# Kernel tuning notes

Measured on AMD Instinct MI355X. Metric: run time of the kernel, lower is better.

## Reference

```python
import jax, jax.numpy as jnp
import numpy as np

N = 100000   # nodes
E = 1600000  # edges
IN_DIM, HID, HEADS, OUT_DIM = 8, 64, 4, 3


def _add_self_loops(src, dst, n):
    loop = jnp.arange(n, dtype=src.dtype)
    return jnp.concatenate([src, loop]), jnp.concatenate([dst, loop])


def gcn_conv(x, src, dst, n, W, b):
    # PyG GCNConv: add self-loops, symmetric normalization deg^-1/2 * deg^-1/2
    s, d = _add_self_loops(src, dst, n)
    deg = jax.ops.segment_sum(jnp.ones(s.shape[0], x.dtype), d, num_segments=n)
    dinv = jnp.where(deg > 0, jax.lax.rsqrt(deg), 0.0)
    norm = dinv[s] * dinv[d]                       # [E']
    h = x @ W                                      # [N, out]
    out = jax.ops.segment_sum(norm[:, None] * h[s], d, num_segments=n)
    return out + b


def gat_conv(x, src, dst, n, W, att_src, att_dst, b):
    # PyG GATConv, concat=True, negative_slope=0.2, self-loops added
    h = (x @ W).reshape(n, HEADS, HID)             # [N, H, C]
    s, d = _add_self_loops(src, dst, n)
    a_src = jnp.sum(h * att_src, axis=-1)          # [N, H]
    a_dst = jnp.sum(h * att_dst, axis=-1)          # [N, H]
    e = jax.nn.leaky_relu(a_src[s] + a_dst[d], negative_slope=0.2)  # [E', H]
    m = jax.lax.stop_gradient(jax.ops.segment_max(e, d, num_segments=n))
    ex = jnp.exp(e - m[d])
    denom = jax.ops.segment_sum(ex, d, num_segments=n)
    alpha = ex / (denom[d] + 1e-16)                # segment softmax over incoming edges
    out = jax.ops.segment_sum(alpha[:, :, None] * h[s], d, num_segments=n)  # [N, H, C]
    return out.reshape(n, HEADS * HID) + b


def setup_inputs() -> dict:
    key = jax.random.key(0)
    ks = jax.random.split(key, 16)
    def glorot(k, shape):
        fan = shape[0] + shape[-1]
        return jax.random.normal(k, shape, jnp.float32) * np.sqrt(2.0 / fan)
    return {
        "x": jax.random.normal(ks[0], (N, IN_DIM), jnp.float32),
        "edge_index": jax.random.randint(ks[1], (2, E), 0, N, jnp.int64 if jax.config.jax_enable_x64 else jnp.int32),
        "w1": glorot(ks[2], (IN_DIM, HID)), "b1": jnp.zeros((HID,), jnp.float32),
        "w2": glorot(ks[3], (HID, HID)),   "b2": jnp.zeros((HID,), jnp.float32),
        "w3": glorot(ks[4], (HID, HID)),   "b3": jnp.zeros((HID,), jnp.float32),
        "wg": glorot(ks[5], (HID, HEADS * HID)), "bg": jnp.zeros((HEADS * HID,), jnp.float32),
        "att_src": glorot(ks[6], (HEADS, HID)),
        "att_dst": glorot(ks[7], (HEADS, HID)),
        "wc1": glorot(ks[8], (HEADS * HID, HID)), "bc1": jnp.zeros((HID,), jnp.float32),
        "wc2": glorot(ks[9], (HID, OUT_DIM)),     "bc2": jnp.zeros((OUT_DIM,), jnp.float32),
    }


def reference(x, edge_index, w1, b1, w2, b2, w3, b3, wg, bg, att_src, att_dst, wc1, bc1, wc2, bc2):
    src, dst = edge_index[0], edge_index[1]
    n = x.shape[0]
    # stacked GCN convs with ReLU; residual when shapes match (layers 2,3)
    h = jax.nn.relu(gcn_conv(x, src, dst, n, w1, b1))
    h = h + jax.nn.relu(gcn_conv(h, src, dst, n, w2, b2))
    h = h + jax.nn.relu(gcn_conv(h, src, dst, n, w3, b3))
    # GAT attention layer (4 heads, concat)
    h_att = gat_conv(h, src, dst, n, wg, att_src, att_dst, bg)  # [N, 256]
    # classifier MLP (dropout is inference no-op)
    z = jax.nn.relu(h_att @ wc1 + bc1)
    logits = z @ wc2 + bc2
    return jax.nn.log_softmax(logits, axis=1)
```

## Files before the change

kernel.cpp:

```cpp
#include <hip/hip_runtime.h>
#include <math.h>


typedef _Float16 half8 __attribute__((ext_vector_type(8)));
typedef _Float16 f16x8 __attribute__((ext_vector_type(8)));
typedef float f32x4 __attribute__((ext_vector_type(4)));

__device__ __forceinline__ float leaky02(float v) { return v > 0.f ? v : 0.2f * v; }


template <int CTRL>
__device__ __forceinline__ float dpp_add(float v) {
    int iv = __builtin_bit_cast(int, v);
    int r = __builtin_amdgcn_update_dpp(iv, iv, CTRL, 0xF, 0xF, false);
    return v + __builtin_bit_cast(float, r);
}
template <int OFF>
__device__ __forceinline__ float swz_add(float v) {
    int r = __builtin_amdgcn_ds_swizzle(__builtin_bit_cast(int, v), OFF);
    return v + __builtin_bit_cast(float, r);
}
template <int CTRL>
__device__ __forceinline__ float dpp_max(float v) {
    int iv = __builtin_bit_cast(int, v);
    int r = __builtin_amdgcn_update_dpp(iv, iv, CTRL, 0xF, 0xF, false);
    return fmaxf(v, __builtin_bit_cast(float, r));
}
template <int OFF>
__device__ __forceinline__ float swz_max(float v) {
    int r = __builtin_amdgcn_ds_swizzle(__builtin_bit_cast(int, v), OFF);
    return fmaxf(v, __builtin_bit_cast(float, r));
}
__device__ __forceinline__ float red8(float v) {
    v = dpp_add<0xB1>(v);
    v = dpp_add<0x4E>(v);
    v = swz_add<0x101F>(v);
    return v;
}
__device__ __forceinline__ float red16(float v) {
    v = dpp_add<0xB1>(v);
    v = dpp_add<0x4E>(v);
    v = swz_add<0x101F>(v);
    v = dpp_add<0x128>(v);
    return v;
}
__device__ __forceinline__ float red64(float v) {
    v = dpp_add<0xB1>(v);
    v = dpp_add<0x4E>(v);
    v = swz_add<0x101F>(v);
    v = dpp_add<0x128>(v);
    v = swz_add<0x401F>(v);
    v = v + __shfl_xor(v, 32);
    return v;
}
__device__ __forceinline__ float red64max(float v) {
    v = dpp_max<0xB1>(v);
    v = dpp_max<0x4E>(v);
    v = swz_max<0x101F>(v);
    v = dpp_max<0x128>(v);
    v = swz_max<0x401F>(v);
    v = fmaxf(v, __shfl_xor(v, 32));
    return v;
}


__global__ void count_kernel(const int* __restrict__ dst, int E, int range,
                             int* __restrict__ counts) {
    int grp = blockIdx.x & 7;
    int nlo = grp * range;
    int nhi = nlo + range;
    int nblk = gridDim.x >> 3;
    int c = blockIdx.x >> 3;
    int stride = nblk * blockDim.x;
    for (int e = c * blockDim.x + threadIdx.x; e < E; e += stride) {
        int d = dst[e];
        if (d >= nlo && d < nhi) atomicAdd(&counts[d], 1);
    }
}

__global__ void scan_pass1(const int* __restrict__ counts, int n, int* __restrict__ blockSums) {
    __shared__ int sh[256];
    int base = blockIdx.x * 2048;
    int tid = threadIdx.x;
    int s = 0;
#pragma unroll
    for (int j = 0; j < 8; ++j) {
        int idx = base + tid * 8 + j;
        if (idx < n) s += counts[idx];
    }
    sh[tid] = s;
    __syncthreads();
    for (int off = 128; off > 0; off >>= 1) {
        if (tid < off) sh[tid] += sh[tid + off];
        __syncthreads();
    }
    if (tid == 0) blockSums[blockIdx.x] = sh[0];
}

__global__ void scan_pass2(const int* __restrict__ blockSums, int nb, int* __restrict__ blockOffs) {
    if (threadIdx.x == 0 && blockIdx.x == 0) {
        int run = 0;
        for (int i = 0; i < nb; ++i) { blockOffs[i] = run; run += blockSums[i]; }
    }
}

__global__ void scan_pass3(const int* __restrict__ counts, int n,
                           const int* __restrict__ blockOffs,
                           const float* __restrict__ x,
                           int* __restrict__ row_ptr, int* __restrict__ cursor,
                           float* __restrict__ dinv, float* __restrict__ rdinv,
                           _Float16* __restrict__ xs) {
    __shared__ int sh[256];
    int base = blockIdx.x * 2048;
    int tid = threadIdx.x;
    int cnt[8];
    int local = 0;
#pragma unroll
    for (int j = 0; j < 8; ++j) {
        int idx = base + tid * 8 + j;
        cnt[j] = (idx < n) ? counts[idx] : 0;
        local += cnt[j];
    }
    sh[tid] = local;
    __syncthreads();
    for (int off = 1; off < 256; off <<= 1) {
        int v = (tid >= off) ? sh[tid - off] : 0;
        __syncthreads();
        sh[tid] += v;
        __syncthreads();
    }
    int run = blockOffs[blockIdx.x] + sh[tid] - local;
#pragma unroll
    for (int j = 0; j < 8; ++j) {
        int idx = base + tid * 8 + j;
        if (idx < n) {
            row_ptr[idx] = run;
            cursor[idx] = run;
            float dv = rsqrtf((float)(cnt[j] + 1));
            dinv[idx] = dv;
            rdinv[idx] = sqrtf((float)(cnt[j] + 1));
#pragma unroll
            for (int t = 0; t < 8; ++t) xs[idx * 8 + t] = (_Float16)(dv * x[idx * 8 + t]);
            run += cnt[j];
            if (idx == n - 1) row_ptr[n] = run;
        }
    }
}

__global__ void scatter_kernel(const int* __restrict__ src, const int* __restrict__ dst,
                               int E, int range,
                               int* __restrict__ cursor, int* __restrict__ col_src) {
    int grp = blockIdx.x & 7;
    int nlo = grp * range;
    int nhi = nlo + range;
    int nblk = gridDim.x >> 3;
    int c = blockIdx.x >> 3;
    int stride = nblk * blockDim.x;
    for (int e = c * blockDim.x + threadIdx.x; e < E; e += stride) {
        int d = dst[e];
        if (d >= nlo && d < nhi) {
            int pos = atomicAdd(&cursor[d], 1);
            col_src[pos] = src[e];
        }
    }
}


__global__ void ccomb_kernel(const float* __restrict__ Wg, const float* __restrict__ bg,
                             const float* __restrict__ wc1, const float* __restrict__ bc1,
                             const float* __restrict__ att_src, const float* __restrict__ att_dst,
                             const float* __restrict__ w2, const float* __restrict__ w3,
                             _Float16* __restrict__ CcombP, float* __restrict__ bcomb,
                             float* __restrict__ wse, float* __restrict__ wde,
                             _Float16* __restrict__ W2P, _Float16* __restrict__ W3P) {
    int bid = blockIdx.x;
    int j = threadIdx.x;
    if (bid < 256) {
        int i = bid;
        float s = 0.f;
        for (int c = 0; c < 64; ++c)
            s += Wg[(i & 63) * 256 + (i >> 6) * 64 + c] * wc1[((i >> 6) * 64 + c) * 64 + j];
        _Float16 hi = (_Float16)s;
        _Float16 lo = (_Float16)(s - (float)hi);
        int kt = i >> 5, l = (((i >> 3) & 3) << 4) | (j & 15), e = i & 7, ct = j >> 4;
        CcombP[(ct * 8 + kt) * 512 + l * 8 + e] = hi;
        CcombP[(32 + ct * 8 + kt) * 512 + l * 8 + e] = lo;
    } else if (bid == 256) {
        float s = bc1[j];
        for (int i = 0; i < 256; ++i) s += bg[i] * wc1[i * 64 + j];
        bcomb[j] = s;
#pragma unroll
        for (int h = 0; h < 4; ++h) {
            float ss = 0.f, sd = 0.f;
            for (int c = 0; c < 64; ++c) {
                float w = Wg[j * 256 + h * 64 + c];
                ss += w * att_src[h * 64 + c];
                sd += w * att_dst[h * 64 + c];
            }
            wse[j * 4 + h] = ss;
            wde[j * 4 + h] = sd;
        }
    } else {
        int i = (bid < 321) ? (bid - 257) : (bid - 321);
        const float* W = (bid < 321) ? w2 : w3;
        _Float16* WP = (bid < 321) ? W2P : W3P;
        float s = W[i * 64 + j];
        _Float16 hi = (_Float16)s;
        _Float16 lo = (_Float16)(s - (float)hi);
        int kt = i >> 5, l = (((i >> 3) & 3) << 4) | (j & 15), e = i & 7, ct = j >> 4;
        WP[(ct * 2 + kt) * 512 + l * 8 + e] = hi;
        WP[(8 + ct * 2 + kt) * 512 + l * 8 + e] = lo;
    }
}


__global__ void gcn_layer1(const half8* __restrict__ xs8,
                           const float* __restrict__ W1, const float* __restrict__ b1,
                           const int* __restrict__ row_ptr, const int* __restrict__ col_src,
                           const float* __restrict__ dinv, int n,
                           _Float16* __restrict__ hs1) {
    int tid = threadIdx.x, lane = tid & 63, wid = tid >> 6;
    int node = blockIdx.x * 4 + wid;
    if (node >= n) return;
    int beg = row_ptr[node], end = row_ptr[node + 1];
    int deg = end - beg;
    float acc[8] = {0.f, 0.f, 0.f, 0.f, 0.f, 0.f, 0.f, 0.f};
    for (int base = 0; base < deg; base += 64) {
        int cs = col_src[min(beg + base + lane, end - 1)];
        half8 v = xs8[cs];
        if (base + lane < deg) {
#pragma unroll
            for (int c = 0; c < 8; ++c) acc[c] += (float)v[c];
        }
    }
#pragma unroll
    for (int c = 0; c < 8; ++c) acc[c] = red64(acc[c]);
    half8 sv = xs8[node];
    float di = dinv[node];
    float agg[8];
#pragma unroll
    for (int c = 0; c < 8; ++c) agg[c] = (acc[c] + (float)sv[c]) * di;
    float sum = b1[lane];
#pragma unroll
    for (int k = 0; k < 8; ++k) sum = fmaf(agg[k], W1[k * 64 + lane], sum);
    hs1[node * 64 + lane] = (_Float16)(di * fmaxf(sum, 0.f));
}


__global__ void gcn_agg(const _Float16* __restrict__ hs_in,
                        const int* __restrict__ row_ptr, const int* __restrict__ col_src,
                        const float* __restrict__ dinv, int n,
                        _Float16* __restrict__ aggout) {
    int tid = threadIdx.x, lane = tid & 63, wid = tid >> 6;
    int node = blockIdx.x * 4 + wid;
    if (node >= n) return;
    int t = lane >> 3, g = lane & 7;
    const half8* hs8 = (const half8*)hs_in;
    int beg = row_ptr[node], end = row_ptr[node + 1];
    int deg = end - beg;
    half8 sv = hs8[node * 8 + t];
    float ac[8];
#pragma unroll
    for (int c = 0; c < 8; ++c) ac[c] = (g == 0) ? (float)sv[c] : 0.f;
    for (int base = 0; base < deg; base += 64) {
        int cs = col_src[min(beg + base + lane, end - 1)];
        int lim = min(deg - base, 64);
        auto bodyF = [&](int eo8) {
            int s = __shfl(cs, eo8 + g);
            half8 v = hs8[s * 8 + t];
#pragma unroll
            for (int c = 0; c < 8; ++c) ac[c] += (float)v[c];
        };
        auto bodyG = [&](int eo8) {
            int eo = eo8 + g;
            int s = __shfl(cs, eo);
            half8 v = hs8[s * 8 + t];
            if (eo < lim) {
#pragma unroll
                for (int c = 0; c < 8; ++c) ac[c] += (float)v[c];
            }
        };
        int eo8 = 0;
        for (; eo8 + 16 <= lim; eo8 += 16) { bodyF(eo8); bodyF(eo8 + 8); }
        if (eo8 < lim) {
            bodyG(eo8);
            eo8 += 8;
            if (eo8 < lim) bodyG(eo8);
        }
    }
    float di = dinv[node];
#pragma unroll
    for (int c = 0; c < 8; ++c) ac[c] = red8(ac[c]) * di;
    if (g == 0) {
        half8 hv;
#pragma unroll
        for (int c = 0; c < 8; ++c) hv[c] = (_Float16)ac[c];
        *(half8*)(aggout + (size_t)node * 64 + t * 8) = hv;
    }
}


template <bool LAST>
__global__ __launch_bounds__(256) void gcn_mfma(
        const _Float16* __restrict__ agg,
        const _Float16* __restrict__ WP,
        const float* __restrict__ b,
        const _Float16* __restrict__ hs_in,
        const float* __restrict__ dinv, const float* __restrict__ rdinv,
        const float* __restrict__ wse, const float* __restrict__ wde,
        int n, _Float16* __restrict__ hout,
        float4* __restrict__ a_src4, float4* __restrict__ a_dst4) {
    __shared__ float partS[4][16][4];
    __shared__ float partD[4][16][4];
    int tid = threadIdx.x;
    int lane = tid & 63;
    int w = __builtin_amdgcn_readfirstlane(tid >> 6);
    int c16 = lane & 15, hi = lane >> 4;

    f16x8 bh[2], blo[2];
#pragma unroll
    for (int kt = 0; kt < 2; ++kt) {
        bh[kt]  = *(const f16x8*)(WP + (size_t)(w * 2 + kt) * 512 + lane * 8);
        blo[kt] = *(const f16x8*)(WP + (size_t)(8 + w * 2 + kt) * 512 + lane * 8);
    }
    int col = w * 16 + c16;
    float bl = b[col];
    float4 wev, wdv;
    if (LAST) {
        wev = ((const float4*)wse)[col];
        wdv = ((const float4*)wde)[col];
    }

    int ntiles = (n + 15) >> 4;
    for (int tile = blockIdx.x; tile < ntiles; tile += gridDim.x) {
        int rowb = tile * 16;
        int arow = min(rowb + c16, n - 1);
        const _Float16* ap = agg + (size_t)arow * 64 + hi * 8;
        f16x8 a0 = *(const f16x8*)(ap);
        f16x8 a1 = *(const f16x8*)(ap + 32);
        f32x4 acc = {0.f, 0.f, 0.f, 0.f};
        acc = __builtin_amdgcn_mfma_f32_16x16x32_f16(a0, bh[0],  acc, 0, 0, 0);
        acc = __builtin_amdgcn_mfma_f32_16x16x32_f16(a0, blo[0], acc, 0, 0, 0);
        acc = __builtin_amdgcn_mfma_f32_16x16x32_f16(a1, bh[1],  acc, 0, 0, 0);
        acc = __builtin_amdgcn_mfma_f32_16x16x32_f16(a1, blo[1], acc, 0, 0, 0);
#pragma unroll
        for (int r = 0; r < 4; ++r) {
            int noder = rowb + hi * 4 + r;
            bool ok = noder < n;
            int ni = min(noder, n - 1);
            float hp = rdinv[ni] * (float)hs_in[(size_t)ni * 64 + col];
            float z = fmaxf(acc[r] + bl, 0.f);
            float hv = hp + z;
            if (!LAST) {
                if (ok) hout[(size_t)ni * 64 + col] = (_Float16)(dinv[ni] * hv);
            } else {
                if (ok) hout[(size_t)ni * 64 + col] = (_Float16)hv;
                float s0 = red16(hv * wev.x), s1 = red16(hv * wev.y);
                float s2 = red16(hv * wev.z), s3 = red16(hv * wev.w);
                float d0 = red16(hv * wdv.x), d1 = red16(hv * wdv.y);
                float d2 = red16(hv * wdv.z), d3 = red16(hv * wdv.w);
                if (c16 == 0) {
                    *(float4*)&partS[w][hi * 4 + r][0] = make_float4(s0, s1, s2, s3);
                    *(float4*)&partD[w][hi * 4 + r][0] = make_float4(d0, d1, d2, d3);
                }
            }
        }
        if (LAST) {
            __syncthreads();
            if (tid < 16) {
                int node = rowb + tid;
                if (node < n) {
                    float4 s = make_float4(
                        partS[0][tid][0] + partS[1][tid][0] + partS[2][tid][0] + partS[3][tid][0],
                        partS[0][tid][1] + partS[1][tid][1] + partS[2][tid][1] + partS[3][tid][1],
                        partS[0][tid][2] + partS[1][tid][2] + partS[2][tid][2] + partS[3][tid][2],
                        partS[0][tid][3] + partS[1][tid][3] + partS[2][tid][3] + partS[3][tid][3]);
                    float4 d = make_float4(
                        partD[0][tid][0] + partD[1][tid][0] + partD[2][tid][0] + partD[3][tid][0],
                        partD[0][tid][1] + partD[1][tid][1] + partD[2][tid][1] + partD[3][tid][1],
                        partD[0][tid][2] + partD[1][tid][2] + partD[2][tid][2] + partD[3][tid][2],
                        partD[0][tid][3] + partD[1][tid][3] + partD[2][tid][3] + partD[3][tid][3]);
                    a_src4[node] = s;
                    a_dst4[node] = d;
                }
            }
            __syncthreads();
        }
    }
}


__global__ __launch_bounds__(256, 4) void gat_agg(
        const _Float16* __restrict__ h3,
        const float4* __restrict__ a_src4, const float4* __restrict__ a_dst4,
        const int* __restrict__ row_ptr, const int* __restrict__ col_src,
        int n, _Float16* __restrict__ aggout) {
    __shared__ _Float16 HsAll[4][32 * 72];
    __shared__ _Float16 wATAll[4][16 * 40];
    int tid = threadIdx.x, lane = tid & 63, wid = tid >> 6;
    int node = blockIdx.x * 4 + wid;
    if (node >= n) return;
    _Float16* Hs = HsAll[wid];
    _Float16* wAT = wATAll[wid];

    int q = lane >> 4, m16 = lane & 15;
    float4 ad = a_dst4[node];
    int beg = row_ptr[node], end = row_ptr[node + 1];
    int deg = end - beg;
    int nslots = deg + 1;

    int swz = q << 4;
    const _Float16* Bb0 = Hs + (size_t)q * 8 * 72 + ((0 * 16 + m16) ^ swz);
    const _Float16* Bb1 = Hs + (size_t)q * 8 * 72 + ((1 * 16 + m16) ^ swz);
    const _Float16* Bb2 = Hs + (size_t)q * 8 * 72 + ((2 * 16 + m16) ^ swz);
    const _Float16* Bb3 = Hs + (size_t)q * 8 * 72 + ((3 * 16 + m16) ^ swz);
    const f16x8* Ab = (const f16x8*)(wAT + m16 * 40 + q * 8);
    int c0 = (lane & 7) * 8;

    f32x4 acc0 = {0.f,0.f,0.f,0.f}, acc1 = {0.f,0.f,0.f,0.f};
    f32x4 acc2 = {0.f,0.f,0.f,0.f}, acc3 = {0.f,0.f,0.f,0.f};
    float dh0 = 0.f, dh1 = 0.f, dh2 = 0.f, dh3 = 0.f;
    float m0 = 0.f, m1 = 0.f, m2 = 0.f, m3 = 0.f;

    for (int base = 0; base < nslots; base += 32) {
        int sl = base + (lane & 31);
        int eidx = max(min(beg + sl - 1, end - 1), 0);
        int cs = (sl == 0) ? node : col_src[eidx];
        float4 as = a_src4[cs];
        float vm = (sl < nslots && lane < 32) ? 1.f : 0.f;
        float l0 = leaky02(as.x + ad.x);
        float l1 = leaky02(as.y + ad.y);
        float l2 = leaky02(as.z + ad.z);
        float l3 = leaky02(as.w + ad.w);
        if (base == 0) {
            m0 = red64max(vm > 0.f ? l0 : -1e30f);
            m1 = red64max(vm > 0.f ? l1 : -1e30f);
            m2 = red64max(vm > 0.f ? l2 : -1e30f);
            m3 = red64max(vm > 0.f ? l3 : -1e30f);
        }
        float w0 = vm * __expf(fminf(l0 - m0, 10.f));
        float w1 = vm * __expf(fminf(l1 - m1, 10.f));
        float w2 = vm * __expf(fminf(l2 - m2, 10.f));
        float w3 = vm * __expf(fminf(l3 - m3, 10.f));
        dh0 += w0; dh1 += w1; dh2 += w2; dh3 += w3;
        if (lane < 32) {
            int s32 = lane & 31;
            _Float16 h0 = (_Float16)w0, h1 = (_Float16)w1;
            _Float16 h2 = (_Float16)w2, h3v = (_Float16)w3;
            wAT[0 * 40 + s32] = h0;
            wAT[1 * 40 + s32] = h1;
            wAT[2 * 40 + s32] = h2;
            wAT[3 * 40 + s32] = h3v;
            wAT[4 * 40 + s32] = (_Float16)(w0 - (float)h0);
            wAT[5 * 40 + s32] = (_Float16)(w1 - (float)h1);
            wAT[6 * 40 + s32] = (_Float16)(w2 - (float)h2);
            wAT[7 * 40 + s32] = (_Float16)(w3 - (float)h3v);
        }
#pragma unroll
        for (int i = 0; i < 4; ++i) {
            int r = i * 8 + (lane >> 3);
            int s = __shfl(cs, r);
            half8 hv = *(const half8*)(h3 + (size_t)s * 64 + c0);
            *(half8*)(Hs + r * 72 + (c0 ^ (i << 4))) = hv;
        }
        __asm__ volatile("s_waitcnt lgkmcnt(0)" ::: "memory");
        f16x8 A = *Ab;
        f16x8 B0, B1, B2, B3;
#pragma unroll
        for (int e = 0; e < 8; ++e) {
            B0[e] = Bb0[e * 72];
            B1[e] = Bb1[e * 72];
            B2[e] = Bb2[e * 72];
            B3[e] = Bb3[e * 72];
        }
        acc0 = __builtin_amdgcn_mfma_f32_16x16x32_f16(A, B0, acc0, 0, 0, 0);
        acc1 = __builtin_amdgcn_mfma_f32_16x16x32_f16(A, B1, acc1, 0, 0, 0);
        acc2 = __builtin_amdgcn_mfma_f32_16x16x32_f16(A, B2, acc2, 0, 0, 0);
        acc3 = __builtin_amdgcn_mfma_f32_16x16x32_f16(A, B3, acc3, 0, 0, 0);
        __asm__ volatile("s_waitcnt lgkmcnt(0)" ::: "memory");
    }

    dh0 = red64(dh0); dh1 = red64(dh1); dh2 = red64(dh2); dh3 = red64(dh3);
    float rd[4];
    rd[0] = 1.f / (dh0 + 1e-16f);
    rd[1] = 1.f / (dh1 + 1e-16f);
    rd[2] = 1.f / (dh2 + 1e-16f);
    rd[3] = 1.f / (dh3 + 1e-16f);
    float tot[4][4];
#pragma unroll
    for (int r = 0; r < 4; ++r) {
        tot[0][r] = acc0[r] + __shfl_xor(acc0[r], 16);
        tot[1][r] = acc1[r] + __shfl_xor(acc1[r], 16);
        tot[2][r] = acc2[r] + __shfl_xor(acc2[r], 16);
        tot[3][r] = acc3[r] + __shfl_xor(acc3[r], 16);
    }
    if (lane < 16) {
        size_t ob = (size_t)node * 256 + lane;
#pragma unroll
        for (int r = 0; r < 4; ++r) {
#pragma unroll
            for (int ct = 0; ct < 4; ++ct)
                aggout[ob + r * 64 + ct * 16] = (_Float16)(tot[ct][r] * rd[r]);
        }
    }
}


__global__ __launch_bounds__(256) void mlp_mfma(
        const _Float16* __restrict__ agg,
        const _Float16* __restrict__ CP,
        const float* __restrict__ bcomb,
        const float* __restrict__ wc2, const float* __restrict__ bc2,
        int n, float* __restrict__ out) {
    __shared__ float part[4][16][3];
    int tid = threadIdx.x;
    int lane = tid & 63;
    int w = __builtin_amdgcn_readfirstlane(tid >> 6);
    int c16 = lane & 15, hi = lane >> 4;

    f16x8 bh[8], blo[8];
#pragma unroll
    for (int kt = 0; kt < 8; ++kt) {
        bh[kt]  = *(const f16x8*)(CP + (size_t)(w * 8 + kt) * 512 + lane * 8);
        blo[kt] = *(const f16x8*)(CP + (size_t)(32 + w * 8 + kt) * 512 + lane * 8);
    }
    int col = w * 16 + c16;
    float bc  = bcomb[col];
    float w20 = wc2[col * 3 + 0], w21 = wc2[col * 3 + 1], w22 = wc2[col * 3 + 2];
    float bb0 = bc2[0], bb1 = bc2[1], bb2 = bc2[2];

    int ntiles = (n + 15) >> 4;
    for (int tile = blockIdx.x; tile < ntiles; tile += gridDim.x) {
        int rowb = tile * 16;
        int row = min(rowb + c16, n - 1);
        const _Float16* ap = agg + (size_t)row * 256 + hi * 8;
        f16x8 a[8];
#pragma unroll
        for (int kt = 0; kt < 8; ++kt) a[kt] = *(const f16x8*)(ap + kt * 32);
        f32x4 acc = {0.f, 0.f, 0.f, 0.f};
#pragma unroll
        for (int kt = 0; kt < 8; ++kt) {
            acc = __builtin_amdgcn_mfma_f32_16x16x32_f16(a[kt], bh[kt],  acc, 0, 0, 0);
            acc = __builtin_amdgcn_mfma_f32_16x16x32_f16(a[kt], blo[kt], acc, 0, 0, 0);
        }
        float pr[4][3];
#pragma unroll
        for (int r = 0; r < 4; ++r) {
            float z = fmaxf(acc[r] + bc, 0.f);
            pr[r][0] = red16(z * w20);
            pr[r][1] = red16(z * w21);
            pr[r][2] = red16(z * w22);
        }
        if (c16 == 0) {
#pragma unroll
            for (int r = 0; r < 4; ++r) {
                part[w][hi * 4 + r][0] = pr[r][0];
                part[w][hi * 4 + r][1] = pr[r][1];
                part[w][hi * 4 + r][2] = pr[r][2];
            }
        }
        __syncthreads();
        if (tid < 16) {
            int node = rowb + tid;
            if (node < n) {
                float e0 = part[0][tid][0] + part[1][tid][0] + part[2][tid][0] + part[3][tid][0] + bb0;
                float e1 = part[0][tid][1] + part[1][tid][1] + part[2][tid][1] + part[3][tid][1] + bb1;
                float e2 = part[0][tid][2] + part[1][tid][2] + part[2][tid][2] + part[3][tid][2] + bb2;
                float mx = fmaxf(e0, fmaxf(e1, e2));
                float lse = mx + logf(expf(e0 - mx) + expf(e1 - mx) + expf(e2 - mx));
                out[(size_t)node * 3 + 0] = e0 - lse;
                out[(size_t)node * 3 + 1] = e1 - lse;
                out[(size_t)node * 3 + 2] = e2 - lse;
            }
        }
        __syncthreads();
    }
}


extern "C" void kernel_launch(void* const* d_in, const int* in_sizes, int n_in,
                              void* d_out, int out_size, void* d_ws, size_t ws_size,
                              hipStream_t stream) {
    const float* x       = (const float*)d_in[0];
    const int*   ei      = (const int*)d_in[1];
    const float* w1      = (const float*)d_in[2];
    const float* b1      = (const float*)d_in[3];
    const float* w2      = (const float*)d_in[4];
    const float* b2      = (const float*)d_in[5];
    const float* w3      = (const float*)d_in[6];
    const float* b3      = (const float*)d_in[7];
    const float* wg      = (const float*)d_in[8];
    const float* bg      = (const float*)d_in[9];
    const float* att_s   = (const float*)d_in[10];
    const float* att_d   = (const float*)d_in[11];
    const float* wc1     = (const float*)d_in[12];
    const float* bc1     = (const float*)d_in[13];
    const float* wc2     = (const float*)d_in[14];
    const float* bc2     = (const float*)d_in[15];
    float* out = (float*)d_out;

    const int N = in_sizes[0] / 8;
    const int E = in_sizes[1] / 2;
    const int* srcv = ei;
    const int* dstv = ei + E;

    char* ws = (char*)d_ws;
    size_t off = 0;
    auto alloc = [&](size_t bytes) -> char* {
        char* p = ws + off;
        off += (bytes + 255) & ~(size_t)255;
        return p;
    };
    int*      counts    = (int*)alloc((size_t)N * 4);
    int*      row_ptr   = (int*)alloc((size_t)(N + 1) * 4);
    int*      cursor    = (int*)alloc((size_t)N * 4);
    int*      col_src   = (int*)alloc((size_t)E * 4);
    int*      blockSums = (int*)alloc(4096 * 4);
    int*      blockOffs = (int*)alloc(4096 * 4);
    float*    dinv      = (float*)alloc((size_t)N * 4);
    float*    rdinv     = (float*)alloc((size_t)N * 4);
    _Float16* xs        = (_Float16*)alloc((size_t)N * 8 * 2);
    float*    a_src     = (float*)alloc((size_t)N * 16);
    float*    a_dst     = (float*)alloc((size_t)N * 16);
    float*    wse       = (float*)alloc(256 * 4);
    float*    wde       = (float*)alloc(256 * 4);
    _Float16* CcombP    = (_Float16*)alloc(64 * 1024);
    float*    bcomb     = (float*)alloc(64 * 4);
    _Float16* W2P       = (_Float16*)alloc(16 * 1024);
    _Float16* W3P       = (_Float16*)alloc(16 * 1024);
    _Float16* bufA      = (_Float16*)alloc((size_t)N * 64 * 2);
    _Float16* bufB      = (_Float16*)alloc((size_t)N * 64 * 2);
    _Float16* aggbuf    = (_Float16*)alloc((size_t)N * 256 * 2);
    _Float16* hs1 = bufA;
    _Float16* hs2 = bufB;
    _Float16* h3  = bufA;
    _Float16* aggA = aggbuf;
    (void)ws_size; (void)n_in; (void)out_size;

    hipMemsetAsync(counts, 0, (size_t)N * 4, stream);

    const int TPB = 256;
    int range = (N + 7) / 8;
    count_kernel<<<1024, TPB, 0, stream>>>(dstv, E, range, counts);

    int NB = (N + 2047) / 2048;
    scan_pass1<<<NB, TPB, 0, stream>>>(counts, N, blockSums);
    scan_pass2<<<1, 64, 0, stream>>>(blockSums, NB, blockOffs);
    scan_pass3<<<NB, TPB, 0, stream>>>(counts, N, blockOffs, x,
                                       row_ptr, cursor, dinv, rdinv, xs);
    scatter_kernel<<<2048, TPB, 0, stream>>>(srcv, dstv, E, range, cursor, col_src);

    ccomb_kernel<<<385, 64, 0, stream>>>(wg, bg, wc1, bc1, att_s, att_d, w2, w3,
                                         CcombP, bcomb, wse, wde, W2P, W3P);

    int gridN = (N + 3) / 4;
    gcn_layer1<<<gridN, TPB, 0, stream>>>((const half8*)xs, w1, b1, row_ptr, col_src,
                                          dinv, N, hs1);

    gcn_agg<<<gridN, TPB, 0, stream>>>(hs1, row_ptr, col_src, dinv, N, aggA);
    gcn_mfma<false><<<2048, TPB, 0, stream>>>(aggA, W2P, b2, hs1, dinv, rdinv,
                                              nullptr, nullptr, N, hs2,
                                              nullptr, nullptr);
    gcn_agg<<<gridN, TPB, 0, stream>>>(hs2, row_ptr, col_src, dinv, N, aggA);
    gcn_mfma<true><<<2048, TPB, 0, stream>>>(aggA, W3P, b3, hs2, dinv, rdinv,
                                             wse, wde, N, h3,
                                             (float4*)a_src, (float4*)a_dst);

    gat_agg<<<gridN, TPB, 0, stream>>>(h3, (const float4*)a_src, (const float4*)a_dst,
                                       row_ptr, col_src, N, aggbuf);
    mlp_mfma<<<2048, TPB, 0, stream>>>(aggbuf, CcombP, bcomb, wc2, bc2, N, out);
}
```

Before: 522.5 us.

## Split GAT aggregation into short and long degree paths with packed waves

Nodes are sorted during the scan into short (degree ≤15) and long lists using atomic counters. A new short-path kernel packs two low-degree nodes into one wave and does a single MFMA pass with no loop. Softmax denominators now come from an extra MFMA against a ones vector instead of a separate cross-lane reduction. The max reduction shrinks to 32 lanes. The cost is an extra launch, a global atomic per node in the scan, and unordered node lists that may hurt locality.

```diff
diff --git a/kernel.cpp b/kernel.cpp
--- a/kernel.cpp
+++ b/kernel.cpp
@@ -42,6 +42,13 @@
     v = dpp_add<0x4E>(v);
     v = swz_add<0x101F>(v);
     v = dpp_add<0x128>(v);
+    return v;
+}
+__device__ __forceinline__ float red16max(float v) {
+    v = dpp_max<0xB1>(v);
+    v = dpp_max<0x4E>(v);
+    v = swz_max<0x101F>(v);
+    v = dpp_max<0x128>(v);
     return v;
 }
 __device__ __forceinline__ float red64(float v) {
@@ -53,13 +60,12 @@
     v = v + __shfl_xor(v, 32);
     return v;
 }
-__device__ __forceinline__ float red64max(float v) {
+__device__ __forceinline__ float red32max(float v) {
     v = dpp_max<0xB1>(v);
     v = dpp_max<0x4E>(v);
     v = swz_max<0x101F>(v);
     v = dpp_max<0x128>(v);
     v = swz_max<0x401F>(v);
-    v = fmaxf(v, __shfl_xor(v, 32));
     return v;
 }
 
@@ -109,7 +115,9 @@
                            const float* __restrict__ x,
                            int* __restrict__ row_ptr, int* __restrict__ cursor,
                            float* __restrict__ dinv, float* __restrict__ rdinv,
-                           _Float16* __restrict__ xs) {
+                           _Float16* __restrict__ xs,
+                           int* __restrict__ shortList, int* __restrict__ longList,
+                           int* __restrict__ nodeCnts) {
     __shared__ int sh[256];
     int base = blockIdx.x * 2048;
     int tid = threadIdx.x;
@@ -141,6 +149,9 @@
             rdinv[idx] = sqrtf((float)(cnt[j] + 1));
 #pragma unroll
             for (int t = 0; t < 8; ++t) xs[idx * 8 + t] = (_Float16)(dv * x[idx * 8 + t]);
+            int isS = (cnt[j] <= 15) ? 0 : 1;
+            int p = atomicAdd(&nodeCnts[isS], 1);
+            if (isS == 0) shortList[p] = idx; else longList[p] = idx;
             run += cnt[j];
             if (idx == n - 1) row_ptr[n] = run;
         }
@@ -390,16 +401,139 @@
 }
 
 
-__global__ __launch_bounds__(256, 4) void gat_agg(
+__global__ __launch_bounds__(256, 4) void gat_agg_short(
         const _Float16* __restrict__ h3,
         const float4* __restrict__ a_src4, const float4* __restrict__ a_dst4,
         const int* __restrict__ row_ptr, const int* __restrict__ col_src,
-        int n, _Float16* __restrict__ aggout) {
+        const int* __restrict__ shortList, const int* __restrict__ nodeCnts,
+        _Float16* __restrict__ aggout) {
     __shared__ _Float16 HsAll[4][32 * 72];
     __shared__ _Float16 wATAll[4][16 * 40];
     int tid = threadIdx.x, lane = tid & 63, wid = tid >> 6;
-    int node = blockIdx.x * 4 + wid;
-    if (node >= n) return;
+    int nshort = nodeCnts[0];
+    int i0 = (blockIdx.x * 4 + wid) * 2;
+    if (i0 >= nshort) return;
+    int nodeA = shortList[i0];
+    int nodeB = (i0 + 1 < nshort) ? shortList[i0 + 1] : nodeA;
+    _Float16* Hs = HsAll[wid];
+    _Float16* wAT = wATAll[wid];
+
+    {
+        int zm = lane >> 2;
+        int zc = ((zm < 8) ? 16 : 0) + (lane & 3) * 4;
+#pragma unroll
+        for (int j = 0; j < 4; ++j) wAT[zm * 40 + zc + j] = (_Float16)0.f;
+    }
+
+    int q = lane >> 4, m16 = lane & 15;
+    int c0 = (lane & 7) * 8;
+    int sl16 = lane & 15;
+    int myNode = (lane < 16) ? nodeA : ((lane < 32) ? nodeB : nodeA);
+    int begL = row_ptr[myNode], endL = row_ptr[myNode + 1];
+    int nslL = endL - begL + 1;
+    float4 adv = a_dst4[myNode];
+    int eidx = max(min(begL + sl16 - 1, endL - 1), 0);
+    int cs = (sl16 == 0) ? myNode : col_src[eidx];
+    float4 as = a_src4[cs];
+    float vm = (sl16 < nslL && lane < 32) ? 1.f : 0.f;
+    float l0 = leaky02(as.x + adv.x);
+    float l1 = leaky02(as.y + adv.y);
+    float l2 = leaky02(as.z + adv.z);
+    float l3 = leaky02(as.w + adv.w);
+    float m0 = red16max(vm > 0.f ? l0 : -1e30f);
+    float m1 = red16max(vm > 0.f ? l1 : -1e30f);
+    float m2 = red16max(vm > 0.f ? l2 : -1e30f);
+    float m3 = red16max(vm > 0.f ? l3 : -1e30f);
+    float w0 = vm * __expf(fminf(l0 - m0, 10.f));
+    float w1 = vm * __expf(fminf(l1 - m1, 10.f));
+    float w2 = vm * __expf(fminf(l2 - m2, 10.f));
+    float w3 = vm * __expf(fminf(l3 - m3, 10.f));
+    if (lane < 32) {
+        int rb = (lane < 16) ? 0 : 8;
+        int k = lane;
+        _Float16 h0 = (_Float16)w0, h1 = (_Float16)w1;
+        _Float16 h2 = (_Float16)w2, h3v = (_Float16)w3;
+        wAT[(rb + 0) * 40 + k] = h0;
+        wAT[(rb + 1) * 40 + k] = h1;
+        wAT[(rb + 2) * 40 + k] = h2;
+        wAT[(rb + 3) * 40 + k] = h3v;
+        wAT[(rb + 4) * 40 + k] = (_Float16)(w0 - (float)h0);
+        wAT[(rb + 5) * 40 + k] = (_Float16)(w1 - (float)h1);
+        wAT[(rb + 6) * 40 + k] = (_Float16)(w2 - (float)h2);
+        wAT[(rb + 7) * 40 + k] = (_Float16)(w3 - (float)h3v);
+    }
+#pragma unroll
+    for (int i = 0; i < 4; ++i) {
+        int r = i * 8 + (lane >> 3);
+        int s = __shfl(cs, r);
+        half8 hv = *(const half8*)(h3 + (size_t)s * 64 + c0);
+        *(half8*)(Hs + r * 72 + (c0 ^ (i << 4))) = hv;
+    }
+    __asm__ volatile("s_waitcnt lgkmcnt(0)" ::: "memory");
+    f16x8 A = *(const f16x8*)(wAT + m16 * 40 + q * 8);
+    int swz = q << 4;
+    const _Float16* Bb0 = Hs + (size_t)q * 8 * 72 + ((0 * 16 + m16) ^ swz);
+    const _Float16* Bb1 = Hs + (size_t)q * 8 * 72 + ((1 * 16 + m16) ^ swz);
+    const _Float16* Bb2 = Hs + (size_t)q * 8 * 72 + ((2 * 16 + m16) ^ swz);
+    const _Float16* Bb3 = Hs + (size_t)q * 8 * 72 + ((3 * 16 + m16) ^ swz);
+    f16x8 B0, B1, B2, B3;
+#pragma unroll
+    for (int e = 0; e < 8; ++e) {
+        B0[e] = Bb0[e * 72];
+        B1[e] = Bb1[e * 72];
+        B2[e] = Bb2[e * 72];
+        B3[e] = Bb3[e * 72];
+    }
+    f16x8 ONES;
+#pragma unroll
+    for (int e = 0; e < 8; ++e) ONES[e] = (_Float16)1.f;
+    f32x4 acc0 = {0.f,0.f,0.f,0.f}, acc1 = {0.f,0.f,0.f,0.f};
+    f32x4 acc2 = {0.f,0.f,0.f,0.f}, acc3 = {0.f,0.f,0.f,0.f};
+    f32x4 accD = {0.f,0.f,0.f,0.f};
+    acc0 = __builtin_amdgcn_mfma_f32_16x16x32_f16(A, B0, acc0, 0, 0, 0);
+    acc1 = __builtin_amdgcn_mfma_f32_16x16x32_f16(A, B1, acc1, 0, 0, 0);
+    acc2 = __builtin_amdgcn_mfma_f32_16x16x32_f16(A, B2, acc2, 0, 0, 0);
+    acc3 = __builtin_amdgcn_mfma_f32_16x16x32_f16(A, B3, acc3, 0, 0, 0);
+    accD = __builtin_amdgcn_mfma_f32_16x16x32_f16(A, ONES, accD, 0, 0, 0);
+
+    float tot[4][4], rdv[4];
+#pragma unroll
+    for (int r = 0; r < 4; ++r) {
+        tot[0][r] = acc0[r] + __shfl_xor(acc0[r], 16);
+        tot[1][r] = acc1[r] + __shfl_xor(acc1[r], 16);
+        tot[2][r] = acc2[r] + __shfl_xor(acc2[r], 16);
+        tot[3][r] = acc3[r] + __shfl_xor(acc3[r], 16);
+        float d = accD[r] + __shfl_xor(accD[r], 16);
+        rdv[r] = 1.f / (d + 1e-16f);
+    }
+    int outNode = -1;
+    if (lane < 16) outNode = nodeA;
+    else if (lane >= 32 && lane < 48 && nodeB != nodeA) outNode = nodeB;
+    if (outNode >= 0) {
+        size_t ob = (size_t)outNode * 256 + (lane & 15);
+#pragma unroll
+        for (int r = 0; r < 4; ++r) {
+#pragma unroll
+            for (int ct = 0; ct < 4; ++ct)
+                aggout[ob + r * 64 + ct * 16] = (_Float16)(tot[ct][r] * rdv[r]);
+        }
+    }
+}
+
+
+__global__ __launch_bounds__(256, 4) void gat_agg_long(
+        const _Float16* __restrict__ h3,
+        const float4* __restrict__ a_src4, const float4* __restrict__ a_dst4,
+        const int* __restrict__ row_ptr, const int* __restrict__ col_src,
+        const int* __restrict__ longList, const int* __restrict__ nodeCnts,
+        _Float16* __restrict__ aggout) {
+    __shared__ _Float16 HsAll[4][32 * 72];
+    __shared__ _Float16 wATAll[4][16 * 40];
+    int tid = threadIdx.x, lane = tid & 63, wid = tid >> 6;
+    int nlong = nodeCnts[1];
+    int li = blockIdx.x * 4 + wid;
+    if (li >= nlong) return;
+    int node = longList[li];
     _Float16* Hs = HsAll[wid];
     _Float16* wAT = wATAll[wid];
 
@@ -408,6 +542,7 @@
     int beg = row_ptr[node], end = row_ptr[node + 1];
     int deg = end - beg;
     int nslots = deg + 1;
+    int c0 = (lane & 7) * 8;
 
     int swz = q << 4;
     const _Float16* Bb0 = Hs + (size_t)q * 8 * 72 + ((0 * 16 + m16) ^ swz);
@@ -415,11 +550,13 @@
     const _Float16* Bb2 = Hs + (size_t)q * 8 * 72 + ((2 * 16 + m16) ^ swz);
     const _Float16* Bb3 = Hs + (size_t)q * 8 * 72 + ((3 * 16 + m16) ^ swz);
     const f16x8* Ab = (const f16x8*)(wAT + m16 * 40 + q * 8);
-    int c0 = (lane & 7) * 8;
+    f16x8 ONES;
+#pragma unroll
+    for (int e = 0; e < 8; ++e) ONES[e] = (_Float16)1.f;
 
     f32x4 acc0 = {0.f,0.f,0.f,0.f}, acc1 = {0.f,0.f,0.f,0.f};
     f32x4 acc2 = {0.f,0.f,0.f,0.f}, acc3 = {0.f,0.f,0.f,0.f};
-    float dh0 = 0.f, dh1 = 0.f, dh2 = 0.f, dh3 = 0.f;
+    f32x4 accD = {0.f,0.f,0.f,0.f};
     float m0 = 0.f, m1 = 0.f, m2 = 0.f, m3 = 0.f;
 
     for (int base = 0; base < nslots; base += 32) {
@@ -433,16 +570,15 @@
         float l2 = leaky02(as.z + ad.z);
         float l3 = leaky02(as.w + ad.w);
         if (base == 0) {
-            m0 = red64max(vm > 0.f ? l0 : -1e30f);
-            m1 = red64max(vm > 0.f ? l1 : -1e30f);
-            m2 = red64max(vm > 0.f ? l2 : -1e30f);
-            m3 = red64max(vm > 0.f ? l3 : -1e30f);
+            m0 = red32max(vm > 0.f ? l0 : -1e30f);
+            m1 = red32max(vm > 0.f ? l1 : -1e30f);
+            m2 = red32max(vm > 0.f ? l2 : -1e30f);
+            m3 = red32max(vm > 0.f ? l3 : -1e30f);
         }
         float w0 = vm * __expf(fminf(l0 - m0, 10.f));
         float w1 = vm * __expf(fminf(l1 - m1, 10.f));
         float w2 = vm * __expf(fminf(l2 - m2, 10.f));
         float w3 = vm * __expf(fminf(l3 - m3, 10.f));
-        dh0 += w0; dh1 += w1; dh2 += w2; dh3 += w3;
         if (lane < 32) {
             int s32 = lane & 31;
             _Float16 h0 = (_Float16)w0, h1 = (_Float16)w1;
@@ -477,22 +613,19 @@
         acc1 = __builtin_amdgcn_mfma_f32_16x16x32_f16(A, B1, acc1, 0, 0, 0);
         acc2 = __builtin_amdgcn_mfma_f32_16x16x32_f16(A, B2, acc2, 0, 0, 0);
         acc3 = __builtin_amdgcn_mfma_f32_16x16x32_f16(A, B3, acc3, 0, 0, 0);
+        accD = __builtin_amdgcn_mfma_f32_16x16x32_f16(A, ONES, accD, 0, 0, 0);
         __asm__ volatile("s_waitcnt lgkmcnt(0)" ::: "memory");
     }
 
-    dh0 = red64(dh0); dh1 = red64(dh1); dh2 = red64(dh2); dh3 = red64(dh3);
-    float rd[4];
-    rd[0] = 1.f / (dh0 + 1e-16f);
-    rd[1] = 1.f / (dh1 + 1e-16f);
-    rd[2] = 1.f / (dh2 + 1e-16f);
-    rd[3] = 1.f / (dh3 + 1e-16f);
-    float tot[4][4];
+    float tot[4][4], rdv[4];
 #pragma unroll
     for (int r = 0; r < 4; ++r) {
         tot[0][r] = acc0[r] + __shfl_xor(acc0[r], 16);
         tot[1][r] = acc1[r] + __shfl_xor(acc1[r], 16);
         tot[2][r] = acc2[r] + __shfl_xor(acc2[r], 16);
         tot[3][r] = acc3[r] + __shfl_xor(acc3[r], 16);
+        float d = accD[r] + __shfl_xor(accD[r], 16);
+        rdv[r] = 1.f / (d + 1e-16f);
     }
     if (lane < 16) {
         size_t ob = (size_t)node * 256 + lane;
@@ -500,7 +633,7 @@
         for (int r = 0; r < 4; ++r) {
 #pragma unroll
             for (int ct = 0; ct < 4; ++ct)
-                aggout[ob + r * 64 + ct * 16] = (_Float16)(tot[ct][r] * rd[r]);
+                aggout[ob + r * 64 + ct * 16] = (_Float16)(tot[ct][r] * rdv[r]);
         }
     }
 }
@@ -628,6 +761,9 @@
     float*    bcomb     = (float*)alloc(64 * 4);
     _Float16* W2P       = (_Float16*)alloc(16 * 1024);
     _Float16* W3P       = (_Float16*)alloc(16 * 1024);
+    int*      shortList = (int*)alloc((size_t)N * 4);
+    int*      longList  = (int*)alloc((size_t)N * 4);
+    int*      nodeCnts  = (int*)alloc(256);
     _Float16* bufA      = (_Float16*)alloc((size_t)N * 64 * 2);
     _Float16* bufB      = (_Float16*)alloc((size_t)N * 64 * 2);
     _Float16* aggbuf    = (_Float16*)alloc((size_t)N * 256 * 2);
@@ -638,6 +774,7 @@
     (void)ws_size; (void)n_in; (void)out_size;
 
     hipMemsetAsync(counts, 0, (size_t)N * 4, stream);
+    hipMemsetAsync(nodeCnts, 0, 8, stream);
 
     const int TPB = 256;
     int range = (N + 7) / 8;
@@ -647,7 +784,8 @@
     scan_pass1<<<NB, TPB, 0, stream>>>(counts, N, blockSums);
     scan_pass2<<<1, 64, 0, stream>>>(blockSums, NB, blockOffs);
     scan_pass3<<<NB, TPB, 0, stream>>>(counts, N, blockOffs, x,
-                                       row_ptr, cursor, dinv, rdinv, xs);
+                                       row_ptr, cursor, dinv, rdinv, xs,
+                                       shortList, longList, nodeCnts);
     scatter_kernel<<<2048, TPB, 0, stream>>>(srcv, dstv, E, range, cursor, col_src);
 
     ccomb_kernel<<<385, 64, 0, stream>>>(wg, bg, wc1, bc1, att_s, att_d, w2, w3,
@@ -666,7 +804,12 @@
                                              wse, wde, N, h3,
                                              (float4*)a_src, (float4*)a_dst);
 
-    gat_agg<<<gridN, TPB, 0, stream>>>(h3, (const float4*)a_src, (const float4*)a_dst,
-                                       row_ptr, col_src, N, aggbuf);
+    int gridS = ((N + 1) / 2 + 3) / 4;
+    gat_agg_short<<<gridS, TPB, 0, stream>>>(h3, (const float4*)a_src,
+                                             (const float4*)a_dst, row_ptr, col_src,
+                                             shortList, nodeCnts, aggbuf);
+    gat_agg_long<<<gridN, TPB, 0, stream>>>(h3, (const float4*)a_src,
+                                            (const float4*)a_dst, row_ptr, col_src,
+                                            longList, nodeCnts, aggbuf);
     mlp_mfma<<<2048, TPB, 0, stream>>>(aggbuf, CcombP, bcomb, wc2, bc2, N, out);
 }
```

Measured after the change: 1.285 ms. 146% more time.
